# Kernel tuning notes

Measured on AMD Instinct MI355X. Metric: run time of the kernel, lower is better.

## Reference

```python
import jax, jax.numpy as jnp
import numpy as np

N_NODES = 100000
N_EDGES = 1600000
IN_CH, HID_CH, LAT = 32, 32, 16


def _gcn_layer(h, W, b, src, dst, norm):
    # PyG GCNConv: h' = scatter_add(norm * (h W)[src] -> dst) + b
    h = h @ W                                   # [N, out]
    msg = h[src] * norm[:, None]                # [E+N, out] gather
    out = jax.ops.segment_sum(msg, dst, num_segments=N_NODES)
    return out + b


def setup_inputs() -> dict:
    key = jax.random.key(0)
    ks = jax.random.split(key, 8)
    x = jax.random.normal(ks[0], (N_NODES, IN_CH), dtype=jnp.float32)
    edge_index = jax.random.randint(ks[1], (2, N_EDGES), 0, N_NODES, dtype=jnp.int32)
    def glorot(k, fan_in, fan_out):
        lim = np.sqrt(6.0 / (fan_in + fan_out)).astype(np.float32)
        return jax.random.uniform(k, (fan_in, fan_out), jnp.float32, -lim, lim)
    return {
        "x": x,
        "edge_index": edge_index,
        "W1": glorot(ks[2], IN_CH, HID_CH),
        "b1": jnp.zeros((HID_CH,), jnp.float32),
        "Wmu": glorot(ks[3], HID_CH, LAT),
        "bmu": jnp.zeros((LAT,), jnp.float32),
        "Wlv": glorot(ks[4], HID_CH, LAT),
        "blv": jnp.zeros((LAT,), jnp.float32),
    }


def reference(x, edge_index, W1, b1, Wmu, bmu, Wlv, blv):
    # Add self-loops (GCNConv default add_self_loops=True)
    loops = jnp.arange(N_NODES, dtype=edge_index.dtype)
    src = jnp.concatenate([edge_index[0], loops])
    dst = jnp.concatenate([edge_index[1], loops])
    # Symmetric normalization: deg over destinations, norm = d^-1/2[src] * d^-1/2[dst]
    deg = jax.ops.segment_sum(jnp.ones_like(dst, dtype=x.dtype), dst,
                              num_segments=N_NODES)
    dinv = jnp.where(deg > 0, jax.lax.rsqrt(deg), 0.0)
    norm = dinv[src] * dinv[dst]                # [E+N]

    h = jax.nn.relu(_gcn_layer(x, W1, b1, src, dst, norm))
    mu = _gcn_layer(h, Wmu, bmu, src, dst, norm)
    logvar = _gcn_layer(h, Wlv, blv, src, dst, norm)
    return (mu, logvar)
```

## Files before the change

### kernel.cpp

```cpp
#include <hip/hip_runtime.h>
#include <hip/hip_fp16.h>

#define N_NODES 100000
#define N_EDGES 1600000
#define NCB 782
#define CAPC 2560
#define P1_BLOCKS 391
#define BKN 128
#define NBF_G 1563


__global__ __launch_bounds__(1024) void k_part1(const int* __restrict__ src,
                                                const int* __restrict__ dst,
                                                int* __restrict__ cursor1,
                                                unsigned* __restrict__ packed1) {
    __shared__ int bh[NCB];
    __shared__ int base[NCB];
    int t = threadIdx.x;
    for (int i = t; i < NCB; i += 1024) bh[i] = 0;
    __syncthreads();
    int g = blockIdx.x * 1024 + t;
    int d[4], s[4], r[4];
    if (g < N_EDGES / 4) {
        int4 d4 = reinterpret_cast<const int4*>(dst)[g];
        int4 s4 = reinterpret_cast<const int4*>(src)[g];
        d[0] = d4.x; d[1] = d4.y; d[2] = d4.z; d[3] = d4.w;
        s[0] = s4.x; s[1] = s4.y; s[2] = s4.z; s[3] = s4.w;
    } else {
        d[0] = d[1] = d[2] = d[3] = -1;
    }
#pragma unroll
    for (int j = 0; j < 4; ++j)
        if (d[j] >= 0) r[j] = atomicAdd(&bh[((unsigned)d[j]) >> 7], 1);
    __syncthreads();
    for (int i = t; i < NCB; i += 1024) {
        int c = bh[i];
        base[i] = i * CAPC + ((c > 0) ? atomicAdd(&cursor1[i], c) : 0);
    }
    __syncthreads();
#pragma unroll
    for (int j = 0; j < 4; ++j) {
        if (d[j] < 0) continue;
        unsigned dd = (unsigned)d[j];
        int b = dd >> 7;
        int pos = base[b] + r[j];
        if (pos < (b + 1) * CAPC)
            packed1[pos] = ((dd & 127u) << 17) | (unsigned)s[j];
    }
}

__global__ __launch_bounds__(512) void k_csrx(const unsigned* __restrict__ packed1,
                                              const int* __restrict__ cursor1,
                                              const float* __restrict__ x,
                                              const float* __restrict__ W1,
                                              unsigned* __restrict__ rowPack,
                                              int* __restrict__ srcSorted,
                                              __half* __restrict__ p1) {
    __shared__ int cnt[BKN];
    __shared__ int scn[BKN];
    __shared__ int stt[BKN];
    __shared__ float sW[1024];
    int t = threadIdx.x;
    int b = blockIdx.x;
    int seg0 = b * CAPC;
    int cc = cursor1[b]; if (cc > CAPC) cc = CAPC;
    int segEnd = seg0 + cc;
    if (t < BKN) cnt[t] = 0;
    for (int i = t; i < 1024; i += 512) sW[i] = W1[i];
    __syncthreads();
    unsigned pk[5]; int rk[5];
    {
        uint4 q = reinterpret_cast<const uint4*>(packed1 + seg0)[t];
        int i0 = seg0 + 4 * t;
        pk[0] = (i0     < segEnd) ? q.x : 0xFFFFFFFFu;
        pk[1] = (i0 + 1 < segEnd) ? q.y : 0xFFFFFFFFu;
        pk[2] = (i0 + 2 < segEnd) ? q.z : 0xFFFFFFFFu;
        pk[3] = (i0 + 3 < segEnd) ? q.w : 0xFFFFFFFFu;
        int i4 = seg0 + 2048 + t;
        pk[4] = (i4 < segEnd) ? packed1[i4] : 0xFFFFFFFFu;
    }
#pragma unroll
    for (int j = 0; j < 5; ++j)
        if (pk[j] != 0xFFFFFFFFu) rk[j] = atomicAdd(&cnt[pk[j] >> 17], 1);
    __syncthreads();
    int v = (t < BKN) ? cnt[t] : 0;
    if (t < BKN) scn[t] = v;
    __syncthreads();
    for (int off = 1; off < BKN; off <<= 1) {
        int u = (t < BKN && t >= off) ? scn[t - off] : 0;
        __syncthreads();
        if (t < BKN) scn[t] += u;
        __syncthreads();
    }
    int node = b * BKN + t;
    if (t < BKN) {
        int start = seg0 + scn[t] - v;
        stt[t] = start;
        if (node < N_NODES) {
            int vc = (v < 2047) ? v : 2047;
            rowPack[node] = (unsigned)start | ((unsigned)vc << 21);
        }
    }
    __syncthreads();
#pragma unroll
    for (int j = 0; j < 5; ++j) {
        if (pk[j] == 0xFFFFFFFFu) continue;
        int pos = stt[pk[j] >> 17] + rk[j];
        srcSorted[pos] = (int)(pk[j] & 0x1FFFFu);
    }
    int lane = t & 31;
    for (int r = (t >> 5); r < BKN; r += 16) {
        int nd = b * BKN + r;
        if (nd > N_NODES) break;
        if (nd == N_NODES) {
            p1[nd * 32 + lane] = __float2half(0.f);
            continue;
        }
        float xv = x[nd * 32 + lane];
        float a = 0.f;
#pragma unroll
        for (int k = 0; k < 32; ++k) {
            float xk = __shfl(xv, k, 32);
            a += xk * sW[k * 32 + lane];
        }
        float di = rsqrtf((float)(cnt[r] + 1));
        p1[nd * 32 + lane] = __float2half(di * a);
    }
}

__device__ __forceinline__ __half2 h2of(const float4& v, int c) {
    return reinterpret_cast<const __half2*>(&v)[c];
}

__device__ __forceinline__ void gatherRow4(const int* __restrict__ srcSorted,
                                           const float4* __restrict__ P,
                                           int beg, int end, int l,
                                           float* __restrict__ acc ) {
    for (int base = beg; base < end; base += 16) {
        int i0 = base + l,      i1 = base + 4 + l;
        int i2 = base + 8 + l,  i3 = base + 12 + l;
        int sA = (i0 < end) ? srcSorted[i0] : N_NODES;
        int sB = (i1 < end) ? srcSorted[i1] : N_NODES;
        int sC = (i2 < end) ? srcSorted[i2] : N_NODES;
        int sD = (i3 < end) ? srcSorted[i3] : N_NODES;
        float4 v0 = P[__shfl(sA, 0, 4) * 4 + l];
        float4 v1 = P[__shfl(sA, 1, 4) * 4 + l];
        float4 v2 = P[__shfl(sA, 2, 4) * 4 + l];
        float4 v3 = P[__shfl(sA, 3, 4) * 4 + l];
        float4 v4 = P[__shfl(sB, 0, 4) * 4 + l];
        float4 v5 = P[__shfl(sB, 1, 4) * 4 + l];
        float4 v6 = P[__shfl(sB, 2, 4) * 4 + l];
        float4 v7 = P[__shfl(sB, 3, 4) * 4 + l];
        float4 v8 = P[__shfl(sC, 0, 4) * 4 + l];
        float4 v9 = P[__shfl(sC, 1, 4) * 4 + l];
        float4 va = P[__shfl(sC, 2, 4) * 4 + l];
        float4 vb = P[__shfl(sC, 3, 4) * 4 + l];
        float4 vc = P[__shfl(sD, 0, 4) * 4 + l];
        float4 vd = P[__shfl(sD, 1, 4) * 4 + l];
        float4 ve = P[__shfl(sD, 2, 4) * 4 + l];
        float4 vf = P[__shfl(sD, 3, 4) * 4 + l];
#pragma unroll
        for (int c = 0; c < 4; ++c) {
            __half2 s01 = __hadd2(h2of(v0, c), h2of(v1, c));
            __half2 s23 = __hadd2(h2of(v2, c), h2of(v3, c));
            __half2 s45 = __hadd2(h2of(v4, c), h2of(v5, c));
            __half2 s67 = __hadd2(h2of(v6, c), h2of(v7, c));
            __half2 s89 = __hadd2(h2of(v8, c), h2of(v9, c));
            __half2 sab = __hadd2(h2of(va, c), h2of(vb, c));
            __half2 scd = __hadd2(h2of(vc, c), h2of(vd, c));
            __half2 sef = __hadd2(h2of(ve, c), h2of(vf, c));
            __half2 sum = __hadd2(__hadd2(__hadd2(s01, s23), __hadd2(s45, s67)),
                                  __hadd2(__hadd2(s89, sab), __hadd2(scd, sef)));
            float2 f = __half22float2(sum);
            acc[2 * c]     += f.x;
            acc[2 * c + 1] += f.y;
        }
    }
}

__global__ __launch_bounds__(256) void k_gx2(const unsigned* __restrict__ rowPack,
                                             const int* __restrict__ srcSorted,
                                             const __half* __restrict__ p1,
                                             const float* __restrict__ b1,
                                             const float* __restrict__ Wmu,
                                             const float* __restrict__ Wlv,
                                             __half* __restrict__ p2) {
    __shared__ float sW[1024];
    __shared__ float sB[32];
    int t = threadIdx.x;
    for (int i = t; i < 1024; i += 256) {
        int k = i >> 5, oc = i & 31;
        sW[i] = (oc < 16) ? Wmu[k * 16 + oc] : Wlv[k * 16 + (oc - 16)];
    }
    if (t < 32) sB[t] = b1[t];
    __syncthreads();
    int l = t & 3;
    int node = blockIdx.x * 64 + (t >> 2);
    if (node > N_NODES) return;
    const float4* P = (const float4*)p1;
    if (node == N_NODES) {
        ((float4*)p2)[node * 4 + l] = make_float4(0.f, 0.f, 0.f, 0.f);
        return;
    }
    unsigned rp = rowPack[node];
    int beg = (int)(rp & 0x1FFFFFu);
    int dg  = (int)(rp >> 21);
    float di = rsqrtf((float)(dg + 1));
    float acc[8] = {0.f, 0.f, 0.f, 0.f, 0.f, 0.f, 0.f, 0.f};
    gatherRow4(srcSorted, P, beg, beg + dg, l, acc);
    float4 ps = P[node * 4 + l];
    float h[8];
#pragma unroll
    for (int c = 0; c < 4; ++c) {
        float2 f = __half22float2(h2of(ps, c));
        h[2 * c]     = fmaxf(di * (acc[2 * c]     + f.x) + sB[8 * l + 2 * c],     0.f);
        h[2 * c + 1] = fmaxf(di * (acc[2 * c + 1] + f.y) + sB[8 * l + 2 * c + 1], 0.f);
    }
    float o[8] = {0.f, 0.f, 0.f, 0.f, 0.f, 0.f, 0.f, 0.f};
    const float4* W4 = (const float4*)sW;
#pragma unroll
    for (int m = 0; m < 4; ++m) {
#pragma unroll
        for (int j = 0; j < 8; ++j) {
            float hk = __shfl(h[j], m, 4);
            int k = 8 * m + j;
            float4 wa = W4[k * 8 + 2 * l];
            float4 wb = W4[k * 8 + 2 * l + 1];
            o[0] += hk * wa.x; o[1] += hk * wa.y; o[2] += hk * wa.z; o[3] += hk * wa.w;
            o[4] += hk * wb.x; o[5] += hk * wb.y; o[6] += hk * wb.z; o[7] += hk * wb.w;
        }
    }
    __half2 r0 = __floats2half2_rn(di * o[0], di * o[1]);
    __half2 r1 = __floats2half2_rn(di * o[2], di * o[3]);
    __half2 r2 = __floats2half2_rn(di * o[4], di * o[5]);
    __half2 r3 = __floats2half2_rn(di * o[6], di * o[7]);
    float4 st;
    st.x = *reinterpret_cast<float*>(&r0);
    st.y = *reinterpret_cast<float*>(&r1);
    st.z = *reinterpret_cast<float*>(&r2);
    st.w = *reinterpret_cast<float*>(&r3);
    ((float4*)p2)[node * 4 + l] = st;
}

__global__ __launch_bounds__(256) void k_gfin(const unsigned* __restrict__ rowPack,
                                              const int* __restrict__ srcSorted,
                                              const __half* __restrict__ p2,
                                              const float* __restrict__ bmu,
                                              const float* __restrict__ blv,
                                              float* __restrict__ out) {
    __shared__ float sB[32];
    int t = threadIdx.x;
    if (t < 32) sB[t] = (t < 16) ? bmu[t] : blv[t - 16];
    __syncthreads();
    int l = t & 3;
    int node = blockIdx.x * 64 + (t >> 2);
    if (node >= N_NODES) return;
    const float4* P = (const float4*)p2;
    unsigned rp = rowPack[node];
    int beg = (int)(rp & 0x1FFFFFu);
    int dg  = (int)(rp >> 21);
    float di = rsqrtf((float)(dg + 1));
    float acc[8] = {0.f, 0.f, 0.f, 0.f, 0.f, 0.f, 0.f, 0.f};
    gatherRow4(srcSorted, P, beg, beg + dg, l, acc);
    float4 ps = P[node * 4 + l];
    float v[8];
#pragma unroll
    for (int c = 0; c < 4; ++c) {
        float2 f = __half22float2(h2of(ps, c));
        v[2 * c]     = di * (acc[2 * c]     + f.x) + sB[8 * l + 2 * c];
        v[2 * c + 1] = di * (acc[2 * c + 1] + f.y) + sB[8 * l + 2 * c + 1];
    }
    float4 o0 = make_float4(v[0], v[1], v[2], v[3]);
    float4 o1 = make_float4(v[4], v[5], v[6], v[7]);
    float4* dst4 = (l < 2) ? (float4*)out
                           : (float4*)(out + (size_t)N_NODES * 16);
    int b4 = node * 4 + (l & 1) * 2;
    dst4[b4]     = o0;
    dst4[b4 + 1] = o1;
}

extern "C" void kernel_launch(void* const* d_in, const int* in_sizes, int n_in,
                              void* d_out, int out_size, void* d_ws, size_t ws_size,
                              hipStream_t stream) {
    const float* x   = (const float*)d_in[0];
    const int*   ei  = (const int*)d_in[1];
    const float* W1  = (const float*)d_in[2];
    const float* b1  = (const float*)d_in[3];
    const float* Wmu = (const float*)d_in[4];
    const float* bmu = (const float*)d_in[5];
    const float* Wlv = (const float*)d_in[6];
    const float* blv = (const float*)d_in[7];
    float* out = (float*)d_out;

    const int* src = ei;
    const int* dst = ei + N_EDGES;

    size_t off = 0;
    int* cursor1 = (int*)d_ws;                          off += NCB;
    unsigned* rowPack = (unsigned*)((int*)d_ws + off);  off += N_NODES;
    off = (off + 63) & ~(size_t)63;
    unsigned* packed1 = (unsigned*)((int*)d_ws + off);  off += (size_t)NCB * CAPC;
    off = (off + 63) & ~(size_t)63;
    int* srcSorted    = (int*)d_ws + off;               off += (size_t)NCB * CAPC;
    off = (off + 63) & ~(size_t)63;
    __half* p1h = (__half*)((int*)d_ws + off);          off += (size_t)(N_NODES + 1) * 16;
    off = (off + 63) & ~(size_t)63;
    __half* p2h = (__half*)((int*)d_ws + off);

    hipMemsetAsync(d_ws, 0, (size_t)NCB * sizeof(int), stream);
    k_part1<<<P1_BLOCKS, 1024, 0, stream>>>(src, dst, cursor1, packed1);
    k_csrx <<<NCB, 512, 0, stream>>>(packed1, cursor1, x, W1,
                                     rowPack, srcSorted, p1h);
    k_gx2  <<<NBF_G, 256, 0, stream>>>(rowPack, srcSorted, p1h,
                                       b1, Wmu, Wlv, p2h);
    k_gfin <<<NBF_G, 256, 0, stream>>>(rowPack, srcSorted, p2h,
                                       bmu, blv, out);
}
```

Before: 181.8 us.

## Split layer-2 features into mu/logvar tables and map halves to XCDs

k_gx2 now writes the mu and logvar halves of the second-layer features into two separate half-precision tables. k_gfin launches twice as many blocks and uses blockIdx&7 so that four XCDs gather only from the mu table and four only from the logvar table. This halves the random-gather working set each XCD's L2 has to hold. The cost is that the CSR indices and rowPack are read twice, and each gathered row becomes a narrower 8-byte load per lane.

After: 186.3 us. 2.5% more time.

```diff
diff --git a/kernel.cpp b/kernel.cpp
--- a/kernel.cpp
+++ b/kernel.cpp
@@ -8,6 +8,7 @@
 #define P1_BLOCKS 391
 #define BKN 128
 #define NBF_G 1563
+#define NFIN_B 3128
 
 
 __global__ __launch_bounds__(1024) void k_part1(const int* __restrict__ src,
@@ -129,6 +130,9 @@
 }
 
 __device__ __forceinline__ __half2 h2of(const float4& v, int c) {
+    return reinterpret_cast<const __half2*>(&v)[c];
+}
+__device__ __forceinline__ __half2 h2of2(const float2& v, int c) {
     return reinterpret_cast<const __half2*>(&v)[c];
 }
 
@@ -178,13 +182,60 @@
     }
 }
 
+__device__ __forceinline__ void gatherRow2(const int* __restrict__ srcSorted,
+                                           const float2* __restrict__ P,
+                                           int beg, int end, int l,
+                                           float* __restrict__ acc ) {
+    for (int base = beg; base < end; base += 16) {
+        int i0 = base + l,      i1 = base + 4 + l;
+        int i2 = base + 8 + l,  i3 = base + 12 + l;
+        int sA = (i0 < end) ? srcSorted[i0] : N_NODES;
+        int sB = (i1 < end) ? srcSorted[i1] : N_NODES;
+        int sC = (i2 < end) ? srcSorted[i2] : N_NODES;
+        int sD = (i3 < end) ? srcSorted[i3] : N_NODES;
+        float2 v0 = P[__shfl(sA, 0, 4) * 4 + l];
+        float2 v1 = P[__shfl(sA, 1, 4) * 4 + l];
+        float2 v2 = P[__shfl(sA, 2, 4) * 4 + l];
+        float2 v3 = P[__shfl(sA, 3, 4) * 4 + l];
+        float2 v4 = P[__shfl(sB, 0, 4) * 4 + l];
+        float2 v5 = P[__shfl(sB, 1, 4) * 4 + l];
+        float2 v6 = P[__shfl(sB, 2, 4) * 4 + l];
+        float2 v7 = P[__shfl(sB, 3, 4) * 4 + l];
+        float2 v8 = P[__shfl(sC, 0, 4) * 4 + l];
+        float2 v9 = P[__shfl(sC, 1, 4) * 4 + l];
+        float2 va = P[__shfl(sC, 2, 4) * 4 + l];
+        float2 vb = P[__shfl(sC, 3, 4) * 4 + l];
+        float2 vc = P[__shfl(sD, 0, 4) * 4 + l];
+        float2 vd = P[__shfl(sD, 1, 4) * 4 + l];
+        float2 ve = P[__shfl(sD, 2, 4) * 4 + l];
+        float2 vf = P[__shfl(sD, 3, 4) * 4 + l];
+#pragma unroll
+        for (int c = 0; c < 2; ++c) {
+            __half2 s01 = __hadd2(h2of2(v0, c), h2of2(v1, c));
+            __half2 s23 = __hadd2(h2of2(v2, c), h2of2(v3, c));
+            __half2 s45 = __hadd2(h2of2(v4, c), h2of2(v5, c));
+            __half2 s67 = __hadd2(h2of2(v6, c), h2of2(v7, c));
+            __half2 s89 = __hadd2(h2of2(v8, c), h2of2(v9, c));
+            __half2 sab = __hadd2(h2of2(va, c), h2of2(vb, c));
+            __half2 scd = __hadd2(h2of2(vc, c), h2of2(vd, c));
+            __half2 sef = __hadd2(h2of2(ve, c), h2of2(vf, c));
+            __half2 sum = __hadd2(__hadd2(__hadd2(s01, s23), __hadd2(s45, s67)),
+                                  __hadd2(__hadd2(s89, sab), __hadd2(scd, sef)));
+            float2 f = __half22float2(sum);
+            acc[2 * c]     += f.x;
+            acc[2 * c + 1] += f.y;
+        }
+    }
+}
+
 __global__ __launch_bounds__(256) void k_gx2(const unsigned* __restrict__ rowPack,
                                              const int* __restrict__ srcSorted,
                                              const __half* __restrict__ p1,
                                              const float* __restrict__ b1,
                                              const float* __restrict__ Wmu,
                                              const float* __restrict__ Wlv,
-                                             __half* __restrict__ p2) {
+                                             __half* __restrict__ p2a,
+                                             __half* __restrict__ p2b) {
     __shared__ float sW[1024];
     __shared__ float sB[32];
     int t = threadIdx.x;
@@ -198,8 +249,9 @@
     int node = blockIdx.x * 64 + (t >> 2);
     if (node > N_NODES) return;
     const float4* P = (const float4*)p1;
+    float4* dstT = (l < 2) ? (float4*)p2a : (float4*)p2b;
     if (node == N_NODES) {
-        ((float4*)p2)[node * 4 + l] = make_float4(0.f, 0.f, 0.f, 0.f);
+        dstT[node * 2 + (l & 1)] = make_float4(0.f, 0.f, 0.f, 0.f);
         return;
     }
     unsigned rp = rowPack[node];
@@ -239,44 +291,43 @@
     st.y = *reinterpret_cast<float*>(&r1);
     st.z = *reinterpret_cast<float*>(&r2);
     st.w = *reinterpret_cast<float*>(&r3);
-    ((float4*)p2)[node * 4 + l] = st;
+    dstT[node * 2 + (l & 1)] = st;
 }
 
 __global__ __launch_bounds__(256) void k_gfin(const unsigned* __restrict__ rowPack,
                                               const int* __restrict__ srcSorted,
-                                              const __half* __restrict__ p2,
+                                              const __half* __restrict__ p2a,
+                                              const __half* __restrict__ p2b,
                                               const float* __restrict__ bmu,
                                               const float* __restrict__ blv,
                                               float* __restrict__ out) {
-    __shared__ float sB[32];
+    __shared__ float sB[16];
     int t = threadIdx.x;
-    if (t < 32) sB[t] = (t < 16) ? bmu[t] : blv[t - 16];
+    int xcd  = blockIdx.x & 7;
+    int half = xcd >> 2;
+    int nb   = (blockIdx.x >> 3) * 4 + (xcd & 3);
+    if (t < 16) sB[t] = half ? blv[t] : bmu[t];
     __syncthreads();
     int l = t & 3;
-    int node = blockIdx.x * 64 + (t >> 2);
+    int node = nb * 64 + (t >> 2);
     if (node >= N_NODES) return;
-    const float4* P = (const float4*)p2;
+    const float2* P = (const float2*)(half ? p2b : p2a);
     unsigned rp = rowPack[node];
     int beg = (int)(rp & 0x1FFFFFu);
     int dg  = (int)(rp >> 21);
     float di = rsqrtf((float)(dg + 1));
-    float acc[8] = {0.f, 0.f, 0.f, 0.f, 0.f, 0.f, 0.f, 0.f};
-    gatherRow4(srcSorted, P, beg, beg + dg, l, acc);
-    float4 ps = P[node * 4 + l];
-    float v[8];
-#pragma unroll
-    for (int c = 0; c < 4; ++c) {
-        float2 f = __half22float2(h2of(ps, c));
-        v[2 * c]     = di * (acc[2 * c]     + f.x) + sB[8 * l + 2 * c];
-        v[2 * c + 1] = di * (acc[2 * c + 1] + f.y) + sB[8 * l + 2 * c + 1];
-    }
-    float4 o0 = make_float4(v[0], v[1], v[2], v[3]);
-    float4 o1 = make_float4(v[4], v[5], v[6], v[7]);
-    float4* dst4 = (l < 2) ? (float4*)out
-                           : (float4*)(out + (size_t)N_NODES * 16);
-    int b4 = node * 4 + (l & 1) * 2;
-    dst4[b4]     = o0;
-    dst4[b4 + 1] = o1;
+    float acc[4] = {0.f, 0.f, 0.f, 0.f};
+    gatherRow2(srcSorted, P, beg, beg + dg, l, acc);
+    float2 ps = P[node * 4 + l];
+    float v[4];
+#pragma unroll
+    for (int c = 0; c < 2; ++c) {
+        float2 f = __half22float2(h2of2(ps, c));
+        v[2 * c]     = di * (acc[2 * c]     + f.x) + sB[4 * l + 2 * c];
+        v[2 * c + 1] = di * (acc[2 * c + 1] + f.y) + sB[4 * l + 2 * c + 1];
+    }
+    ((float4*)out)[(size_t)half * N_NODES * 4 + (size_t)node * 4 + l] =
+        make_float4(v[0], v[1], v[2], v[3]);
 }
 
 extern "C" void kernel_launch(void* const* d_in, const int* in_sizes, int n_in,
@@ -305,14 +356,16 @@
     off = (off + 63) & ~(size_t)63;
     __half* p1h = (__half*)((int*)d_ws + off);          off += (size_t)(N_NODES + 1) * 16;
     off = (off + 63) & ~(size_t)63;
-    __half* p2h = (__half*)((int*)d_ws + off);
+    __half* p2a = (__half*)((int*)d_ws + off);          off += (size_t)(N_NODES + 1) * 8;
+    off = (off + 63) & ~(size_t)63;
+    __half* p2b = (__half*)((int*)d_ws + off);
 
     hipMemsetAsync(d_ws, 0, (size_t)NCB * sizeof(int), stream);
     k_part1<<<P1_BLOCKS, 1024, 0, stream>>>(src, dst, cursor1, packed1);
     k_csrx <<<NCB, 512, 0, stream>>>(packed1, cursor1, x, W1,
                                      rowPack, srcSorted, p1h);
     k_gx2  <<<NBF_G, 256, 0, stream>>>(rowPack, srcSorted, p1h,
-                                       b1, Wmu, Wlv, p2h);
-    k_gfin <<<NBF_G, 256, 0, stream>>>(rowPack, srcSorted, p2h,
-                                       bmu, blv, out);
-}
+                                       b1, Wmu, Wlv, p2a, p2b);
+    k_gfin <<<NFIN_B, 256, 0, stream>>>(rowPack, srcSorted, p2a, p2b,
+                                        bmu, blv, out);
+}
```
